# Kernel optimization log

Hardware: AMD Instinct MI355X
Metric: run time of the kernel (lower is better)

## Reference

```python
import jax, jax.numpy as jnp
import numpy as np

B, C, H, W = 8, 512, 128, 128   # batch, ham_channels, feature-map H, W
S, R = 1, 64                    # md_s, md_r
EVAL_STEPS = 7
EPS = 1e-6


def conv1x1(x, w, b):
    # x: [B,C,H,W], w: [O,C] (1x1 conv kernel), b: [O]
    return jnp.einsum('bchw,oc->bohw', x, w) + b[None, :, None, None]


def _update_coef(x, bases, coef):
    # x: [B,D,N], bases: [B,D,R], coef: [B,N,R]
    num = jnp.einsum('bdn,bdr->bnr', x, bases)
    btb = jnp.einsum('bdr,bds->brs', bases, bases)          # [B,R,R]
    den = jnp.einsum('bnr,brs->bns', coef, btb)
    return coef * num / (den + EPS)


def nmf2d(x, bases):
    # Multiplicative-update NMF, eval path (inv_t = 1).
    coef = jax.nn.softmax(jnp.einsum('bdn,bdr->bnr', x, bases), axis=-1)

    def step(carry, _):
        bases, coef = carry
        coef = _update_coef(x, bases, coef)
        num = jnp.einsum('bdn,bnr->bdr', x, coef)
        ctc = jnp.einsum('bnr,bns->brs', coef, coef)        # [B,R,R]
        den = jnp.einsum('bdr,brs->bds', bases, ctc)
        bases = bases * num / (den + EPS)
        return (bases, coef), None

    (bases, coef), _ = jax.lax.scan(step, (bases, coef), None, length=EVAL_STEPS)
    coef = _update_coef(x, bases, coef)                      # compute_coef
    return jnp.einsum('bdr,bnr->bdn', bases, coef)           # bases @ coef^T


def setup_inputs() -> dict:
    key = jax.random.key(0)
    ks = jax.random.split(key, 5)
    x = jax.random.normal(ks[0], (B, C, H, W), jnp.float32)
    w_in = jax.random.normal(ks[1], (C, C), jnp.float32) * 0.02
    b_in = jnp.zeros((C,), jnp.float32)
    w_out = jax.random.normal(ks[2], (C, C), jnp.float32) * 0.02
    b_out = jnp.zeros((C,), jnp.float32)
    bases = jax.random.uniform(ks[3], (S, C // S, R), jnp.float32)
    # f.normalize(..., dim=1): L2-normalize over channel dim
    bases = bases / jnp.maximum(jnp.linalg.norm(bases, axis=1, keepdims=True), 1e-12)
    return {'x': x, 'w_in': w_in, 'b_in': b_in, 'w_out': w_out, 'b_out': b_out, 'bases': bases}


def reference(x, w_in, b_in, w_out, b_out, bases):
    # ham_in (1x1 conv) + relu
    h = jax.nn.relu(conv1x1(x, w_in, b_in))
    # NMF2D: view to [B*s, C/s, H*W], repeat bases over batch
    xf = h.reshape(B * S, C // S, H * W)
    bb = jnp.tile(bases, (B, 1, 1))                          # [B*s, C/s, R]
    y = nmf2d(xf, bb).reshape(B, C, H, W)
    # ham_out (1x1 conv, no norm) + residual relu
    y = conv1x1(y, w_out, b_out)
    return jax.nn.relu(x + y)
```

## Files before the change

### kernel.cpp

```cpp
#include <hip/hip_runtime.h>

#define B_ 8
#define C_ 512
#define N_ 16384
#define R_ 64
#define EPS 1e-6f

typedef float  f32x4  __attribute__((ext_vector_type(4)));
typedef short  bf16x4 __attribute__((ext_vector_type(4)));
typedef short  bf16x8 __attribute__((ext_vector_type(8)));

#define DI __device__ __forceinline__

DI short f2bf(float f) {
    union { float f; unsigned u; } a; a.f = f;
    unsigned r = a.u + 0x7fffu + ((a.u >> 16) & 1u);
    return (short)(r >> 16);
}
DI float bf2f(short s) {
    union { unsigned u; float f; } a;
    a.u = ((unsigned)(unsigned short)s) << 16;
    return a.f;
}

union BV { bf16x8 v; bf16x4 h[2]; };
DI bf16x8 ldfrag(const short* p) {
    BV u;
    u.h[0] = *(const bf16x4*)p;
    u.h[1] = *(const bf16x4*)(p + 4);
    return u.v;
}
DI f32x4 mfma16(bf16x8 a, bf16x8 b, f32x4 c) {
    return __builtin_amdgcn_mfma_f32_16x16x32_bf16(a, b, c, 0, 0, 0);
}

__global__ __launch_bounds__(256)
void k_prep(const float* __restrict__ bases, float* __restrict__ basesT,
            short* __restrict__ basesTb) {
    int idx = blockIdx.x * 256 + threadIdx.x;
    const int d = idx & 511;
    const int r = (idx >> 9) & 63;
    const float v = bases[d * 64 + r];
    basesT[idx]  = v;
    basesTb[idx] = f2bf(v);
}

__global__ __launch_bounds__(256)
void k_conv1(const float* __restrict__ W, const float* __restrict__ bias,
             const float* __restrict__ X, short* __restrict__ H) {
    const int nb = blockIdx.x * 128, mb = blockIdx.y * 128, bb = blockIdx.z;
    const float* Xb = X + (size_t)bb * C_ * N_;
    short* Hb = H + (size_t)bb * C_ * N_;
    __shared__ short As[128 * 36];
    __shared__ short Bs[128 * 36];
    const int t = threadIdx.x;
    const int lane = t & 63, wave = t >> 6;
    const int wm = wave >> 1, wn = wave & 1;
    const int fr = lane & 15, fg = lane >> 4;
    f32x4 zero4 = {0.f, 0.f, 0.f, 0.f};
    f32x4 acc[4][4];
    for (int i = 0; i < 4; i++) for (int j = 0; j < 4; j++) acc[i][j] = zero4;

    for (int kb = 0; kb < C_; kb += 32) {
        {
            const int row = t >> 1, kh = (t & 1) * 16;
            const float* src = W + (size_t)(mb + row) * C_ + kb + kh;
            short* dst = &As[row * 36 + kh];
#pragma unroll
            for (int i = 0; i < 4; i++) {
                float4 v = *(const float4*)(src + 4 * i);
                bf16x4 s; s[0]=f2bf(v.x); s[1]=f2bf(v.y); s[2]=f2bf(v.z); s[3]=f2bf(v.w);
                *(bf16x4*)(dst + 4 * i) = s;
            }
        }
        {
            const int n0 = (t & 31) * 4;
#pragma unroll
            for (int i = 0; i < 2; i++) {
                const int kp = (t >> 5) + 8 * i, k = 2 * kp;
                const float* r0 = Xb + (size_t)(kb + k) * N_ + nb + n0;
                float4 va = *(const float4*)r0;
                float4 vb = *(const float4*)(r0 + N_);
                const float* pa = (const float*)&va;
                const float* pb = (const float*)&vb;
#pragma unroll
                for (int j = 0; j < 4; j++) {
                    unsigned lo = (unsigned short)f2bf(pa[j]);
                    unsigned hi = (unsigned short)f2bf(pb[j]);
                    *(unsigned*)&Bs[(n0 + j) * 36 + k] = lo | (hi << 16);
                }
            }
        }
        __syncthreads();
        bf16x8 af[4], bv[4];
#pragma unroll
        for (int mi = 0; mi < 4; mi++) af[mi] = ldfrag(&As[(wm * 64 + mi * 16 + fr) * 36 + fg * 8]);
#pragma unroll
        for (int ni = 0; ni < 4; ni++) bv[ni] = ldfrag(&Bs[(wn * 64 + ni * 16 + fr) * 36 + fg * 8]);
#pragma unroll
        for (int mi = 0; mi < 4; mi++)
#pragma unroll
            for (int ni = 0; ni < 4; ni++)
                acc[mi][ni] = mfma16(af[mi], bv[ni], acc[mi][ni]);
        __syncthreads();
    }
#pragma unroll
    for (int mi = 0; mi < 4; mi++) {
#pragma unroll
        for (int j = 0; j < 4; j++) {
            const int m = mb + wm * 64 + mi * 16 + fg * 4 + j;
            const float bvv = bias[m];
            short* orow = Hb + (size_t)m * N_ + nb;
#pragma unroll
            for (int ni = 0; ni < 4; ni++) {
                float v = acc[mi][ni][j] + bvv;
                v = v > 0.f ? v : 0.f;
                orow[wn * 64 + ni * 16 + fr] = f2bf(v);
            }
        }
    }
}

template<int UPDATE>
__global__ __launch_bounds__(256)
void k_coef(const short* __restrict__ basesTb, const short* __restrict__ Hh,
            const short* __restrict__ btb, short* __restrict__ coef) {
    const int nb = blockIdx.x * 256, bb = blockIdx.y;
    const short* Hb = Hh + (size_t)bb * C_ * N_;
    const short* bT = basesTb + (size_t)bb * R_ * C_;
    short* coefB = coef + (size_t)bb * R_ * N_;
    __shared__ short As[64 * 36];
    __shared__ short Bs[256 * 36];
    __shared__ short Ds[64 * 68];
    const int t = threadIdx.x;
    const int lane = t & 63, wave = t >> 6;
    const int fr = lane & 15, fg = lane >> 4;
    f32x4 zero4 = {0.f, 0.f, 0.f, 0.f};
    f32x4 accN[4][4];
    for (int i = 0; i < 4; i++) for (int j = 0; j < 4; j++) accN[i][j] = zero4;

    for (int kb = 0; kb < C_; kb += 32) {
        {
            const int row = t >> 2, kc = (t & 3) * 8;
            const short* src = bT + row * C_ + kb + kc;
            short* dst = &As[row * 36 + kc];
            *(bf16x4*)dst = *(const bf16x4*)src;
            *(bf16x4*)(dst + 4) = *(const bf16x4*)(src + 4);
        }
        {
            const int n0 = (t & 63) * 4;
#pragma unroll
            for (int i = 0; i < 4; i++) {
                const int kp = (t >> 6) + 4 * i, k = 2 * kp;
                const short* r0 = Hb + (size_t)(kb + k) * N_ + nb + n0;
                bf16x4 a = *(const bf16x4*)r0;
                bf16x4 b = *(const bf16x4*)(r0 + N_);
#pragma unroll
                for (int j = 0; j < 4; j++)
                    *(unsigned*)&Bs[(n0 + j) * 36 + k] =
                        (unsigned)(unsigned short)a[j] | ((unsigned)(unsigned short)b[j] << 16);
            }
        }
        __syncthreads();
        bf16x8 af[4], bv[4];
#pragma unroll
        for (int mi = 0; mi < 4; mi++) af[mi] = ldfrag(&As[(mi * 16 + fr) * 36 + fg * 8]);
#pragma unroll
        for (int ni = 0; ni < 4; ni++) bv[ni] = ldfrag(&Bs[(wave * 64 + ni * 16 + fr) * 36 + fg * 8]);
#pragma unroll
        for (int mi = 0; mi < 4; mi++)
#pragma unroll
            for (int ni = 0; ni < 4; ni++)
                accN[mi][ni] = mfma16(af[mi], bv[ni], accN[mi][ni]);
        __syncthreads();
    }

    f32x4 accD[4][4];
    if (UPDATE) {
        for (int i = 0; i < 4; i++) for (int j = 0; j < 4; j++) accD[i][j] = zero4;
        {
            const short* bt = btb + bb * R_ * R_;
#pragma unroll
            for (int i = 0; i < 2; i++) {
                const int row = t & 63, kc8 = ((t >> 6) + 4 * i) * 8;
                const short* src = bt + row * 64 + kc8;
                short* dst = &Ds[row * 68 + kc8];
                *(bf16x4*)dst = *(const bf16x4*)src;
                *(bf16x4*)(dst + 4) = *(const bf16x4*)(src + 4);
            }
        }
        for (int ks = 0; ks < 2; ks++) {
            const int n0 = (t & 63) * 4;
#pragma unroll
            for (int i = 0; i < 4; i++) {
                const int kp = (t >> 6) + 4 * i, k = 2 * kp;
                const short* r0 = coefB + (size_t)(ks * 32 + k) * N_ + nb + n0;
                bf16x4 a = *(const bf16x4*)r0;
                bf16x4 b = *(const bf16x4*)(r0 + N_);
#pragma unroll
                for (int j = 0; j < 4; j++)
                    *(unsigned*)&Bs[(n0 + j) * 36 + k] =
                        (unsigned)(unsigned short)a[j] | ((unsigned)(unsigned short)b[j] << 16);
            }
            __syncthreads();
            bf16x8 af[4], bv[4];
#pragma unroll
            for (int mi = 0; mi < 4; mi++) af[mi] = ldfrag(&Ds[(mi * 16 + fr) * 68 + ks * 32 + fg * 8]);
#pragma unroll
            for (int ni = 0; ni < 4; ni++) bv[ni] = ldfrag(&Bs[(wave * 64 + ni * 16 + fr) * 36 + fg * 8]);
#pragma unroll
            for (int mi = 0; mi < 4; mi++)
#pragma unroll
                for (int ni = 0; ni < 4; ni++)
                    accD[mi][ni] = mfma16(af[mi], bv[ni], accD[mi][ni]);
            __syncthreads();
        }
#pragma unroll
        for (int mi = 0; mi < 4; mi++)
#pragma unroll
            for (int ni = 0; ni < 4; ni++)
#pragma unroll
                for (int j = 0; j < 4; j++) {
                    const int m = mi * 16 + fg * 4 + j;
                    const int n = nb + wave * 64 + ni * 16 + fr;
                    short* p = coefB + (size_t)m * N_ + n;
                    float oldv = bf2f(*p);
                    float nv = oldv * accN[mi][ni][j] / (accD[mi][ni][j] + EPS);
                    *p = f2bf(nv);
                }
    } else {
#pragma unroll
        for (int ni = 0; ni < 4; ni++) {
            float mx = -3e38f;
#pragma unroll
            for (int mi = 0; mi < 4; mi++)
#pragma unroll
                for (int j = 0; j < 4; j++) mx = fmaxf(mx, accN[mi][ni][j]);
            mx = fmaxf(mx, __shfl_xor(mx, 16, 64));
            mx = fmaxf(mx, __shfl_xor(mx, 32, 64));
            float sm = 0.f;
#pragma unroll
            for (int mi = 0; mi < 4; mi++)
#pragma unroll
                for (int j = 0; j < 4; j++) {
                    float e = __expf(accN[mi][ni][j] - mx);
                    accN[mi][ni][j] = e;
                    sm += e;
                }
            sm += __shfl_xor(sm, 16, 64);
            sm += __shfl_xor(sm, 32, 64);
            const float inv = 1.f / sm;
#pragma unroll
            for (int mi = 0; mi < 4; mi++)
#pragma unroll
                for (int j = 0; j < 4; j++) {
                    const int m = mi * 16 + fg * 4 + j;
                    const int n = nb + wave * 64 + ni * 16 + fr;
                    coefB[(size_t)m * N_ + n] = f2bf(accN[mi][ni][j] * inv);
                }
        }
    }
}

template<int MODE>
__global__ __launch_bounds__(256)
void k_tn(const short* __restrict__ coef, const short* __restrict__ Hh,
          const short* __restrict__ basesTb, const float* __restrict__ Wout,
          float* __restrict__ parts, short* __restrict__ btb, short* __restrict__ wf) {
    const int ddt = blockIdx.x, ch = blockIdx.y, bb = blockIdx.z;
    const int kLen = (MODE == 0) ? 2048 : 512;
    const int k0g = ch * kLen;
    const short* Ap; int lda;
    if (MODE == 0) { Ap = coef + (size_t)bb * R_ * N_; lda = N_; }
    else           { Ap = basesTb + (size_t)bb * R_ * C_; lda = C_; }
    __shared__ short As[64 * 72];
    __shared__ short Bs[64 * 72];
    const int t = threadIdx.x;
    const int lane = t & 63, wave = t >> 6;
    const int fr = lane & 15, fg = lane >> 4;
    f32x4 zero4 = {0.f, 0.f, 0.f, 0.f};
    f32x4 acc[4];
    for (int i = 0; i < 4; i++) acc[i] = zero4;

    for (int kb = 0; kb < kLen; kb += 64) {
#pragma unroll
        for (int i = 0; i < 2; i++) {
            const int kg = (t & 7) * 8, row = (t >> 3) + 32 * i;
            const short* src = Ap + (size_t)row * lda + k0g + kb + kg;
            short* dst = &As[row * 72 + kg];
            *(bf16x4*)dst = *(const bf16x4*)src;
            *(bf16x4*)(dst + 4) = *(const bf16x4*)(src + 4);
        }
#pragma unroll
        for (int i = 0; i < 2; i++) {
            const int kg = (t & 7) * 8, row = (t >> 3) + 32 * i;
            const int dd = ddt * 64 + row;
            short* dst = &Bs[row * 72 + kg];
            if (MODE == 2) {
                const float* src = Wout + (size_t)dd * C_ + kb + kg;
                float4 v0 = *(const float4*)src;
                float4 v1 = *(const float4*)(src + 4);
                bf16x4 s0, s1;
                s0[0]=f2bf(v0.x); s0[1]=f2bf(v0.y); s0[2]=f2bf(v0.z); s0[3]=f2bf(v0.w);
                s1[0]=f2bf(v1.x); s1[1]=f2bf(v1.y); s1[2]=f2bf(v1.z); s1[3]=f2bf(v1.w);
                *(bf16x4*)dst = s0; *(bf16x4*)(dst + 4) = s1;
            } else {
                const short* src;
                if (MODE == 0)
                    src = (dd < C_) ? Hh + (size_t)bb * C_ * N_ + (size_t)dd * N_ + k0g + kb + kg
                                    : coef + (size_t)bb * R_ * N_ + (size_t)(dd - C_) * N_ + k0g + kb + kg;
                else
                    src = basesTb + (size_t)bb * R_ * C_ + (size_t)dd * C_ + kb + kg;
                *(bf16x4*)dst = *(const bf16x4*)src;
                *(bf16x4*)(dst + 4) = *(const bf16x4*)(src + 4);
            }
        }
        __syncthreads();
#pragma unroll
        for (int kk = 0; kk < 2; kk++) {
            bf16x8 a = ldfrag(&As[(wave * 16 + fr) * 72 + kk * 32 + fg * 8]);
#pragma unroll
            for (int ni = 0; ni < 4; ni++) {
                bf16x8 b = ldfrag(&Bs[(ni * 16 + fr) * 72 + kk * 32 + fg * 8]);
                acc[ni] = mfma16(a, b, acc[ni]);
            }
        }
        __syncthreads();
    }
#pragma unroll
    for (int ni = 0; ni < 4; ni++)
#pragma unroll
        for (int j = 0; j < 4; j++) {
            const int r = wave * 16 + fg * 4 + j;
            const int dd = ddt * 64 + ni * 16 + fr;
            if (MODE == 0)
                parts[(((size_t)bb * 8 + ch) * 64 + r) * 576 + dd] = acc[ni][j];
            else if (MODE == 1)
                btb[bb * R_ * R_ + r * 64 + dd] = f2bf(acc[ni][j]);
            else
                wf[(size_t)bb * C_ * R_ + (size_t)dd * 64 + r] = f2bf(acc[ni][j]);
        }
}

__global__ __launch_bounds__(256)
void k_bases_update(const float* __restrict__ parts, float* __restrict__ basesT,
                    short* __restrict__ basesTb) {
    const int dt = blockIdx.x, bb = blockIdx.y;
    __shared__ float ctcL[64 * 64];
    const int t = threadIdx.x;
    for (int idx = t; idx < 4096; idx += 256) {
        const int r = idx >> 6, s = idx & 63;
        float sum = 0.f;
#pragma unroll
        for (int ch = 0; ch < 8; ch++)
            sum += parts[(((size_t)bb * 8 + ch) * 64 + r) * 576 + 512 + s];
        ctcL[idx] = sum;
    }
    __syncthreads();
    float nv[16];
#pragma unroll
    for (int i = 0; i < 16; i++) {
        const int idx = t + i * 256;
        const int r = idx >> 6, d = dt * 64 + (idx & 63);
        float num = 0.f;
#pragma unroll
        for (int ch = 0; ch < 8; ch++)
            num += parts[(((size_t)bb * 8 + ch) * 64 + r) * 576 + d];
        float den = 0.f;
        const float* bcol = basesT + (size_t)bb * R_ * C_ + d;
        for (int s = 0; s < 64; s++)
            den += ctcL[r * 64 + s] * bcol[(size_t)s * C_];
        const float oldv = basesT[(size_t)bb * R_ * C_ + (size_t)r * C_ + d];
        nv[i] = oldv * num / (den + EPS);
    }
    __syncthreads();
#pragma unroll
    for (int i = 0; i < 16; i++) {
        const int idx = t + i * 256;
        const int r = idx >> 6, d = dt * 64 + (idx & 63);
        basesT[(size_t)bb * R_ * C_ + (size_t)r * C_ + d] = nv[i];
        basesTb[(size_t)bb * R_ * C_ + (size_t)r * C_ + d] = f2bf(nv[i]);
    }
}

__global__ __launch_bounds__(256)
void k_final(const short* __restrict__ wf, const short* __restrict__ coef,
             const float* __restrict__ X, const float* __restrict__ bias,
             float* __restrict__ out) {
    const int nb = blockIdx.x * 128, mb = blockIdx.y * 128, bb = blockIdx.z;
    __shared__ short As[128 * 72];
    __shared__ short Bs[128 * 72];
    const int t = threadIdx.x;
    const int lane = t & 63, wave = t >> 6;
    const int wm = wave >> 1, wn = wave & 1;
    const int fr = lane & 15, fg = lane >> 4;
    const short* wfb = wf + (size_t)bb * C_ * R_;
    const short* coefB = coef + (size_t)bb * R_ * N_;
    f32x4 zero4 = {0.f, 0.f, 0.f, 0.f};
    f32x4 acc[4][4];
    for (int i = 0; i < 4; i++) for (int j = 0; j < 4; j++) acc[i][j] = zero4;

#pragma unroll
    for (int i = 0; i < 4; i++) {
        const int kg = (t & 7) * 8, row = (t >> 3) + 32 * i;
        const short* src = wfb + (size_t)(mb + row) * 64 + kg;
        short* dst = &As[row * 72 + kg];
        *(bf16x4*)dst = *(const bf16x4*)src;
        *(bf16x4*)(dst + 4) = *(const bf16x4*)(src + 4);
    }
    {
        const int n0 = (t & 31) * 4;
#pragma unroll
        for (int i = 0; i < 4; i++) {
            const int kp = (t >> 5) + 8 * i, k = 2 * kp;
            const short* r0 = coefB + (size_t)k * N_ + nb + n0;
            bf16x4 a = *(const bf16x4*)r0;
            bf16x4 b = *(const bf16x4*)(r0 + N_);
#pragma unroll
            for (int j = 0; j < 4; j++)
                *(unsigned*)&Bs[(n0 + j) * 72 + k] =
                    (unsigned)(unsigned short)a[j] | ((unsigned)(unsigned short)b[j] << 16);
        }
    }
    __syncthreads();
#pragma unroll
    for (int kk = 0; kk < 2; kk++) {
        bf16x8 af[4], bv[4];
#pragma unroll
        for (int mi = 0; mi < 4; mi++) af[mi] = ldfrag(&As[(wm * 64 + mi * 16 + fr) * 72 + kk * 32 + fg * 8]);
#pragma unroll
        for (int ni = 0; ni < 4; ni++) bv[ni] = ldfrag(&Bs[(wn * 64 + ni * 16 + fr) * 72 + kk * 32 + fg * 8]);
#pragma unroll
        for (int mi = 0; mi < 4; mi++)
#pragma unroll
            for (int ni = 0; ni < 4; ni++)
                acc[mi][ni] = mfma16(af[mi], bv[ni], acc[mi][ni]);
    }
    const float* Xb = X + (size_t)bb * C_ * N_;
    float* Ob = out + (size_t)bb * C_ * N_;
#pragma unroll
    for (int mi = 0; mi < 4; mi++)
#pragma unroll
        for (int j = 0; j < 4; j++) {
            const int m = mb + wm * 64 + mi * 16 + fg * 4 + j;
            const float bvv = bias[m];
            const float* xrow = Xb + (size_t)m * N_ + nb;
            float* orow = Ob + (size_t)m * N_ + nb;
#pragma unroll
            for (int ni = 0; ni < 4; ni++) {
                const int n = wn * 64 + ni * 16 + fr;
                float v = xrow[n] + acc[mi][ni][j] + bvv;
                orow[n] = v > 0.f ? v : 0.f;
            }
        }
}

extern "C" void kernel_launch(void* const* d_in, const int* in_sizes, int n_in,
                              void* d_out, int out_size, void* d_ws, size_t ws_size,
                              hipStream_t stream) {
    const float* x     = (const float*)d_in[0];
    const float* w_in  = (const float*)d_in[1];
    const float* b_in  = (const float*)d_in[2];
    const float* w_out = (const float*)d_in[3];
    const float* b_out = (const float*)d_in[4];
    const float* bases = (const float*)d_in[5];
    float* out = (float*)d_out;

    short* h       = (short*)d_ws;
    short* coef    = h + (size_t)67108864;
    float* basesT  = (float*)(coef + 8388608);
    short* basesTb = (short*)(basesT + 262144);
    short* btb     = basesTb + 262144;
    short* wf      = btb + 32768;
    float* parts   = (float*)(wf + 262144);

    k_prep<<<1024, 256, 0, stream>>>(bases, basesT, basesTb);
    k_conv1<<<dim3(128, 4, 8), 256, 0, stream>>>(w_in, b_in, x, h);
    k_coef<0><<<dim3(64, 8), 256, 0, stream>>>(basesTb, h, btb, coef);
    for (int s = 0; s < 7; s++) {
        k_tn<1><<<dim3(1, 1, 8), 256, 0, stream>>>(coef, h, basesTb, w_out, parts, btb, wf);
        k_coef<1><<<dim3(64, 8), 256, 0, stream>>>(basesTb, h, btb, coef);
        k_tn<0><<<dim3(9, 8, 8), 256, 0, stream>>>(coef, h, basesTb, w_out, parts, btb, wf);
        k_bases_update<<<dim3(8, 8), 256, 0, stream>>>(parts, basesT, basesTb);
    }
    k_tn<1><<<dim3(1, 1, 8), 256, 0, stream>>>(coef, h, basesTb, w_out, parts, btb, wf);
    k_coef<1><<<dim3(64, 8), 256, 0, stream>>>(basesTb, h, btb, coef);
    k_tn<2><<<dim3(8, 1, 8), 256, 0, stream>>>(coef, h, basesTb, w_out, parts, btb, wf);
    k_final<<<dim3(128, 4, 8), 256, 0, stream>>>(wf, coef, x, b_out, out);
}
```

Before: 1.512 ms.

## Pre-convert w_in to bf16, remap global-to-LDS transpose loads, shrink LDS padding

```diff
diff --git a/kernel.cpp b/kernel.cpp
--- a/kernel.cpp
+++ b/kernel.cpp
@@ -1,4 +1,5 @@
 #include <hip/hip_runtime.h>
+#include <hip/hip_bf16.h>
 
 #define B_ 8
 #define C_ 512
@@ -21,6 +22,11 @@
     union { unsigned u; float f; } a;
     a.u = ((unsigned)(unsigned short)s) << 16;
     return a.f;
+}
+DI unsigned pk2(float lo, float hi) {
+    union { __hip_bfloat162 h; unsigned u; } c;
+    c.h = __float22bfloat162_rn(make_float2(lo, hi));
+    return c.u;
 }
 
 union BV { bf16x8 v; bf16x4 h[2]; };
@@ -36,17 +42,19 @@
 
 __global__ __launch_bounds__(256)
 void k_prep(const float* __restrict__ bases, float* __restrict__ basesT,
-            short* __restrict__ basesTb) {
+            short* __restrict__ basesTb, const float* __restrict__ w_in,
+            short* __restrict__ wbf) {
     int idx = blockIdx.x * 256 + threadIdx.x;
     const int d = idx & 511;
     const int r = (idx >> 9) & 63;
     const float v = bases[d * 64 + r];
     basesT[idx]  = v;
     basesTb[idx] = f2bf(v);
-}
-
-__global__ __launch_bounds__(256)
-void k_conv1(const float* __restrict__ W, const float* __restrict__ bias,
+    wbf[idx] = f2bf(w_in[idx]);
+}
+
+__global__ __launch_bounds__(256)
+void k_conv1(const short* __restrict__ Wbf, const float* __restrict__ bias,
              const float* __restrict__ X, short* __restrict__ H) {
     const int nb = blockIdx.x * 128, mb = blockIdx.y * 128, bb = blockIdx.z;
     const float* Xb = X + (size_t)bb * C_ * N_;
@@ -61,34 +69,27 @@
     f32x4 acc[4][4];
     for (int i = 0; i < 4; i++) for (int j = 0; j < 4; j++) acc[i][j] = zero4;
 
+    const int an_row = t >> 2, an_kc = (t & 3) * 8;
+    const int bn = t & 15, bkp = t >> 4;
+
     for (int kb = 0; kb < C_; kb += 32) {
         {
-            const int row = t >> 1, kh = (t & 1) * 16;
-            const float* src = W + (size_t)(mb + row) * C_ + kb + kh;
-            short* dst = &As[row * 36 + kh];
-#pragma unroll
-            for (int i = 0; i < 4; i++) {
-                float4 v = *(const float4*)(src + 4 * i);
-                bf16x4 s; s[0]=f2bf(v.x); s[1]=f2bf(v.y); s[2]=f2bf(v.z); s[3]=f2bf(v.w);
-                *(bf16x4*)(dst + 4 * i) = s;
+#pragma unroll
+            for (int i = 0; i < 2; i++) {
+                const int row = an_row + 64 * i;
+                const short* src = Wbf + (size_t)(mb + row) * C_ + kb + an_kc;
+                short* dst = &As[row * 36 + an_kc];
+                *(bf16x4*)dst = *(const bf16x4*)src;
+                *(bf16x4*)(dst + 4) = *(const bf16x4*)(src + 4);
             }
         }
         {
-            const int n0 = (t & 31) * 4;
-#pragma unroll
-            for (int i = 0; i < 2; i++) {
-                const int kp = (t >> 5) + 8 * i, k = 2 * kp;
-                const float* r0 = Xb + (size_t)(kb + k) * N_ + nb + n0;
-                float4 va = *(const float4*)r0;
-                float4 vb = *(const float4*)(r0 + N_);
-                const float* pa = (const float*)&va;
-                const float* pb = (const float*)&vb;
-#pragma unroll
-                for (int j = 0; j < 4; j++) {
-                    unsigned lo = (unsigned short)f2bf(pa[j]);
-                    unsigned hi = (unsigned short)f2bf(pb[j]);
-                    *(unsigned*)&Bs[(n0 + j) * 36 + k] = lo | (hi << 16);
-                }
+            const float* r0 = Xb + (size_t)(kb + 2 * bkp) * N_ + nb + bn;
+#pragma unroll
+            for (int p = 0; p < 8; p++) {
+                const float va = r0[16 * p];
+                const float vb = r0[16 * p + N_];
+                *(unsigned*)&Bs[(bn + 16 * p) * 36 + 2 * bkp] = pk2(va, vb);
             }
         }
         __syncthreads();
@@ -139,6 +140,8 @@
     f32x4 accN[4][4];
     for (int i = 0; i < 4; i++) for (int j = 0; j < 4; j++) accN[i][j] = zero4;
 
+    const int bn = 2 * (t & 15), bkp = t >> 4;
+
     for (int kb = 0; kb < C_; kb += 32) {
         {
             const int row = t >> 2, kc = (t & 3) * 8;
@@ -148,17 +151,13 @@
             *(bf16x4*)(dst + 4) = *(const bf16x4*)(src + 4);
         }
         {
-            const int n0 = (t & 63) * 4;
-#pragma unroll
-            for (int i = 0; i < 4; i++) {
-                const int kp = (t >> 6) + 4 * i, k = 2 * kp;
-                const short* r0 = Hb + (size_t)(kb + k) * N_ + nb + n0;
-                bf16x4 a = *(const bf16x4*)r0;
-                bf16x4 b = *(const bf16x4*)(r0 + N_);
-#pragma unroll
-                for (int j = 0; j < 4; j++)
-                    *(unsigned*)&Bs[(n0 + j) * 36 + k] =
-                        (unsigned)(unsigned short)a[j] | ((unsigned)(unsigned short)b[j] << 16);
+            const short* r0 = Hb + (size_t)(kb + 2 * bkp) * N_ + nb + bn;
+#pragma unroll
+            for (int p = 0; p < 8; p++) {
+                const unsigned ra = *(const unsigned*)(r0 + 32 * p);
+                const unsigned rb = *(const unsigned*)(r0 + 32 * p + N_);
+                *(unsigned*)&Bs[(bn + 32 * p) * 36 + 2 * bkp] = (ra & 0xffffu) | (rb << 16);
+                *(unsigned*)&Bs[(bn + 1 + 32 * p) * 36 + 2 * bkp] = (ra >> 16) | (rb & 0xffff0000u);
             }
         }
         __syncthreads();
@@ -190,17 +189,13 @@
             }
         }
         for (int ks = 0; ks < 2; ks++) {
-            const int n0 = (t & 63) * 4;
-#pragma unroll
-            for (int i = 0; i < 4; i++) {
-                const int kp = (t >> 6) + 4 * i, k = 2 * kp;
-                const short* r0 = coefB + (size_t)(ks * 32 + k) * N_ + nb + n0;
-                bf16x4 a = *(const bf16x4*)r0;
-                bf16x4 b = *(const bf16x4*)(r0 + N_);
-#pragma unroll
-                for (int j = 0; j < 4; j++)
-                    *(unsigned*)&Bs[(n0 + j) * 36 + k] =
-                        (unsigned)(unsigned short)a[j] | ((unsigned)(unsigned short)b[j] << 16);
+            const short* r0 = coefB + (size_t)(ks * 32 + 2 * bkp) * N_ + nb + bn;
+#pragma unroll
+            for (int p = 0; p < 8; p++) {
+                const unsigned ra = *(const unsigned*)(r0 + 32 * p);
+                const unsigned rb = *(const unsigned*)(r0 + 32 * p + N_);
+                *(unsigned*)&Bs[(bn + 32 * p) * 36 + 2 * bkp] = (ra & 0xffffu) | (rb << 16);
+                *(unsigned*)&Bs[(bn + 1 + 32 * p) * 36 + 2 * bkp] = (ra >> 16) | (rb & 0xffff0000u);
             }
             __syncthreads();
             bf16x8 af[4], bv[4];
@@ -273,8 +268,8 @@
     const short* Ap; int lda;
     if (MODE == 0) { Ap = coef + (size_t)bb * R_ * N_; lda = N_; }
     else           { Ap = basesTb + (size_t)bb * R_ * C_; lda = C_; }
-    __shared__ short As[64 * 72];
-    __shared__ short Bs[64 * 72];
+    __shared__ short As[64 * 68];
+    __shared__ short Bs[64 * 68];
     const int t = threadIdx.x;
     const int lane = t & 63, wave = t >> 6;
     const int fr = lane & 15, fg = lane >> 4;
@@ -287,7 +282,7 @@
         for (int i = 0; i < 2; i++) {
             const int kg = (t & 7) * 8, row = (t >> 3) + 32 * i;
             const short* src = Ap + (size_t)row * lda + k0g + kb + kg;
-            short* dst = &As[row * 72 + kg];
+            short* dst = &As[row * 68 + kg];
             *(bf16x4*)dst = *(const bf16x4*)src;
             *(bf16x4*)(dst + 4) = *(const bf16x4*)(src + 4);
         }
@@ -295,15 +290,15 @@
         for (int i = 0; i < 2; i++) {
             const int kg = (t & 7) * 8, row = (t >> 3) + 32 * i;
             const int dd = ddt * 64 + row;
-            short* dst = &Bs[row * 72 + kg];
+            short* dst = &Bs[row * 68 + kg];
             if (MODE == 2) {
                 const float* src = Wout + (size_t)dd * C_ + kb + kg;
                 float4 v0 = *(const float4*)src;
                 float4 v1 = *(const float4*)(src + 4);
-                bf16x4 s0, s1;
-                s0[0]=f2bf(v0.x); s0[1]=f2bf(v0.y); s0[2]=f2bf(v0.z); s0[3]=f2bf(v0.w);
-                s1[0]=f2bf(v1.x); s1[1]=f2bf(v1.y); s1[2]=f2bf(v1.z); s1[3]=f2bf(v1.w);
-                *(bf16x4*)dst = s0; *(bf16x4*)(dst + 4) = s1;
+                *(unsigned*)dst = pk2(v0.x, v0.y);
+                *(unsigned*)(dst + 2) = pk2(v0.z, v0.w);
+                *(unsigned*)(dst + 4) = pk2(v1.x, v1.y);
+                *(unsigned*)(dst + 6) = pk2(v1.z, v1.w);
             } else {
                 const short* src;
                 if (MODE == 0)
@@ -318,10 +313,10 @@
         __syncthreads();
 #pragma unroll
         for (int kk = 0; kk < 2; kk++) {
-            bf16x8 a = ldfrag(&As[(wave * 16 + fr) * 72 + kk * 32 + fg * 8]);
+            bf16x8 a = ldfrag(&As[(wave * 16 + fr) * 68 + kk * 32 + fg * 8]);
 #pragma unroll
             for (int ni = 0; ni < 4; ni++) {
-                bf16x8 b = ldfrag(&Bs[(ni * 16 + fr) * 72 + kk * 32 + fg * 8]);
+                bf16x8 b = ldfrag(&Bs[(ni * 16 + fr) * 68 + kk * 32 + fg * 8]);
                 acc[ni] = mfma16(a, b, acc[ni]);
             }
         }
@@ -388,8 +383,8 @@
              const float* __restrict__ X, const float* __restrict__ bias,
              float* __restrict__ out) {
     const int nb = blockIdx.x * 128, mb = blockIdx.y * 128, bb = blockIdx.z;
-    __shared__ short As[128 * 72];
-    __shared__ short Bs[128 * 72];
+    __shared__ short As[128 * 68];
+    __shared__ short Bs[128 * 68];
     const int t = threadIdx.x;
     const int lane = t & 63, wave = t >> 6;
     const int wm = wave >> 1, wn = wave & 1;
@@ -404,22 +399,23 @@
     for (int i = 0; i < 4; i++) {
         const int kg = (t & 7) * 8, row = (t >> 3) + 32 * i;
         const short* src = wfb + (size_t)(mb + row) * 64 + kg;
-        short* dst = &As[row * 72 + kg];
+        short* dst = &As[row * 68 + kg];
         *(bf16x4*)dst = *(const bf16x4*)src;
         *(bf16x4*)(dst + 4) = *(const bf16x4*)(src + 4);
     }
     {
-        const int n0 = (t & 31) * 4;
-#pragma unroll
-        for (int i = 0; i < 4; i++) {
-            const int kp = (t >> 5) + 8 * i, k = 2 * kp;
-            const short* r0 = coefB + (size_t)k * N_ + nb + n0;
-            bf16x4 a = *(const bf16x4*)r0;
-            bf16x4 b = *(const bf16x4*)(r0 + N_);
-#pragma unroll
-            for (int j = 0; j < 4; j++)
-                *(unsigned*)&Bs[(n0 + j) * 72 + k] =
-                    (unsigned)(unsigned short)a[j] | ((unsigned)(unsigned short)b[j] << 16);
+        const int bn = 2 * (t & 15), bkp = t >> 4;
+#pragma unroll
+        for (int i = 0; i < 2; i++) {
+            const int kp = bkp + 16 * i;
+            const short* r0 = coefB + (size_t)(2 * kp) * N_ + nb + bn;
+#pragma unroll
+            for (int p = 0; p < 4; p++) {
+                const unsigned ra = *(const unsigned*)(r0 + 32 * p);
+                const unsigned rb = *(const unsigned*)(r0 + 32 * p + N_);
+                *(unsigned*)&Bs[(bn + 32 * p) * 68 + 2 * kp] = (ra & 0xffffu) | (rb << 16);
+                *(unsigned*)&Bs[(bn + 1 + 32 * p) * 68 + 2 * kp] = (ra >> 16) | (rb & 0xffff0000u);
+            }
         }
     }
     __syncthreads();
@@ -427,9 +423,9 @@
     for (int kk = 0; kk < 2; kk++) {
         bf16x8 af[4], bv[4];
 #pragma unroll
-        for (int mi = 0; mi < 4; mi++) af[mi] = ldfrag(&As[(wm * 64 + mi * 16 + fr) * 72 + kk * 32 + fg * 8]);
-#pragma unroll
-        for (int ni = 0; ni < 4; ni++) bv[ni] = ldfrag(&Bs[(wn * 64 + ni * 16 + fr) * 72 + kk * 32 + fg * 8]);
+        for (int mi = 0; mi < 4; mi++) af[mi] = ldfrag(&As[(wm * 64 + mi * 16 + fr) * 68 + kk * 32 + fg * 8]);
+#pragma unroll
+        for (int ni = 0; ni < 4; ni++) bv[ni] = ldfrag(&Bs[(wn * 64 + ni * 16 + fr) * 68 + kk * 32 + fg * 8]);
 #pragma unroll
         for (int mi = 0; mi < 4; mi++)
 #pragma unroll
@@ -473,9 +469,10 @@
     short* btb     = basesTb + 262144;
     short* wf      = btb + 32768;
     float* parts   = (float*)(wf + 262144);
-
-    k_prep<<<1024, 256, 0, stream>>>(bases, basesT, basesTb);
-    k_conv1<<<dim3(128, 4, 8), 256, 0, stream>>>(w_in, b_in, x, h);
+    short* wbf     = (short*)(parts + 2359296);
+
+    k_prep<<<1024, 256, 0, stream>>>(bases, basesT, basesTb, w_in, wbf);
+    k_conv1<<<dim3(128, 4, 8), 256, 0, stream>>>(wbf, b_in, x, h);
     k_coef<0><<<dim3(64, 8), 256, 0, stream>>>(basesTb, h, btb, coef);
     for (int s = 0; s < 7; s++) {
         k_tn<1><<<dim3(1, 1, 8), 256, 0, stream>>>(coef, h, basesTb, w_out, parts, btb, wf);
```

After: 1.473 ms. 1.03x faster.
